# Kernel optimization log

Measured on AMD Instinct MI355X. Metric: run time of the kernel, lower is better.

## Reference

```python
import jax, jax.numpy as jnp
import numpy as np

# Config constants (MLAConfig)
B, S = 1, 2048                 # batch, context_len (prefill: seq == context_len)
H = 16                         # num_heads
DN, DR, DV = 128, 64, 128      # qk_nope_head_dim, qk_rope_head_dim, v_head_dim
QL, C = 1536, 512              # q_lora_rank, kv_lora_rank
BLK = 128                      # fp8 dequant block size
MAX_CACHE = 4096
SOFTMAX_SCALE = 1.0 / np.sqrt(DN + DR)  # 1/sqrt(192)
NEG_INF = -10000.0


def gen_rope(n_total, head_size):
    # theta_j = 10000^{-2j/d}; idx_theta[i, 0, :] = [i*theta, i*theta] (repeated halves)
    theta = 1.0 / (10000.0 ** (jnp.arange(0, head_size, 2, dtype=jnp.float32) / head_size))
    idx = jnp.outer(jnp.arange(n_total, dtype=jnp.float32), theta)  # (N, d/2)
    return jnp.tile(idx[:, None, :], (1, 1, 2))                     # (N, 1, d)


def fp8_dequant(x, s, block=BLK):
    # Block-wise dequant: x (M,N) * per-(block x block) scale s (M/b, N/b).
    M, N = x.shape
    m, n = M // block, N // block  # shapes chosen divisible by block -> no padding
    return (x.reshape(m, block, n, block) * s[:, None, :, None]).reshape(M, N)


def apply_rope(x, cos, sin):
    # x: (B*S, heads, d). Interleaved RoPE: de-interleave pairs into halves,
    # then x*cos + rotate_half(x)*sin with cos/sin (B*S, 1, d).
    bs, h, d = x.shape
    x = x.reshape(bs, h, d // 2, 2).transpose(0, 1, 3, 2).reshape(bs, h, d)
    rot = jnp.concatenate([-x[..., d // 2:], x[..., :d // 2]], axis=-1)
    return x * cos + rot * sin


def setup_inputs() -> dict:
    key = jax.random.key(0)
    ks = jax.random.split(key, 9)
    WUQ = jax.random.normal(ks[0], (H * (DN + DR), QL), dtype=jnp.float32)
    WUKV = jax.random.normal(ks[1], (H * (DN + DV), C), dtype=jnp.float32)
    # positive, small block scales so attention logits stay well-conditioned
    WUQ_scale = 0.05 * jax.random.uniform(ks[2], (H * (DN + DR) // BLK, QL // BLK), dtype=jnp.float32)
    WUKV_scale = 0.05 * jax.random.uniform(ks[3], (H * (DN + DV) // BLK, C // BLK), dtype=jnp.float32)
    Q = jax.random.normal(ks[4], (B, S, QL), dtype=jnp.float32)
    KV = jax.random.normal(ks[5], (B, S, C), dtype=jnp.float32)
    PE = jax.random.normal(ks[6], (B, S, DR), dtype=jnp.float32)
    kv_cache = jax.random.normal(ks[7], (B, MAX_CACHE, C), dtype=jnp.float32)
    pe_cache = jax.random.normal(ks[8], (B, MAX_CACHE, DR), dtype=jnp.float32)
    idx_theta = gen_rope(B * S, DR)
    mask = jnp.triu(jnp.full((S, S), NEG_INF, dtype=jnp.float32), k=1)
    return {"WUQ": WUQ, "WUQ_scale": WUQ_scale, "WUKV": WUKV, "WUKV_scale": WUKV_scale,
            "Q": Q, "KV": KV, "PE": PE, "kv_cache": kv_cache, "pe_cache": pe_cache,
            "idx_theta": idx_theta, "mask": mask}


def reference(WUQ, WUQ_scale, WUKV, WUKV_scale, Q, KV, PE, kv_cache, pe_cache, idx_theta, mask):
    bsz, seqlen, _ = Q.shape
    # fp8 block-wise dequant of the low-rank up-projection weights
    WUQd = fp8_dequant(WUQ, WUQ_scale)
    WUKVd = fp8_dequant(WUKV, WUKV_scale)
    # Q up-projection from q_lora latent: (B*S, QL) @ (QL, H*(DN+DR))
    q = (Q.reshape(-1, QL) @ WUQd.T).reshape(bsz, seqlen, H, DN + DR)
    q_nope, q_pe = q[..., :DN], q[..., DN:]
    cos, sin = jnp.cos(idx_theta), jnp.sin(idx_theta)  # (B*S, 1, DR)
    q_pe = apply_rope(q_pe.reshape(bsz * seqlen, H, DR), cos, sin).reshape(bsz, seqlen, H, DR)
    k_pe = apply_rope(PE.reshape(bsz * seqlen, 1, DR), cos, sin).reshape(bsz, seqlen, DR)
    # absorbed low-rank K matrix: q_nope projected into the kv latent space
    W3 = WUKVd.reshape(H, DN + DV, C)
    q_lat = jnp.einsum('bshd,hdc->bshc', q_nope, W3[:, :DN])
    # continuous-cache prefill: write fresh latents into the cache, attend over them
    kv = kv_cache.at[:, :seqlen].set(KV)[:, :seqlen]   # (B, S, C)
    pe = pe_cache.at[:, :seqlen].set(k_pe)[:, :seqlen]  # (B, S, DR)
    scores = (jnp.einsum('bshc,btc->bsht', q_lat, kv)
              + jnp.einsum('bshr,btr->bsht', q_pe, pe)) * SOFTMAX_SCALE
    scores = scores + mask[None, :, None, :]
    attn = jax.nn.softmax(scores, axis=-1)
    x = jnp.einsum('bsht,btc->bshc', attn, kv)
    out = jnp.einsum('bshc,hdc->bshd', x, W3[:, DN:])  # V up-projection (absorbed)
    return out  # (B, S, H, DV)
```

## Files before the change

kernel.cpp:

```cpp
#include <hip/hip_runtime.h>

typedef __bf16 bf16_t;
typedef __attribute__((ext_vector_type(4))) __bf16 bf16x4;
typedef __attribute__((ext_vector_type(8))) __bf16 bf16x8;
typedef __attribute__((ext_vector_type(4))) float f32x4;

#define SOFTMAX_SCALE 0.07216878364870322f
#define NEG_MASK (-10000.0f)
#define NEG_BIG  (-1e30f)

__device__ __forceinline__ void async16(const bf16_t* g, bf16_t* l) {
  __builtin_amdgcn_global_load_lds(
      (const __attribute__((address_space(1))) unsigned int*)g,
      (__attribute__((address_space(3))) unsigned int*)l, 16, 0, 0);
}


__global__ void k_rope_tables(const float* __restrict__ idxt,
                              float* __restrict__ cost, float* __restrict__ sint) {
  int i = blockIdx.x * 256 + threadIdx.x;
  float a = idxt[i];
  cost[i] = cosf(a);
  sint[i] = sinf(a);
}

__global__ void k_dequant(const float* __restrict__ W, const float* __restrict__ S,
                          bf16_t* __restrict__ out, int cols, int scols) {
  int i = (blockIdx.x * 256 + threadIdx.x) * 4;
  int r = i / cols, c = i % cols;
  float s = S[(r >> 7) * scols + (c >> 7)];
  float4 w = *(const float4*)(W + i);
  out[i + 0] = (bf16_t)(w.x * s);
  out[i + 1] = (bf16_t)(w.y * s);
  out[i + 2] = (bf16_t)(w.z * s);
  out[i + 3] = (bf16_t)(w.w * s);
}

__global__ void k_wv1t(const bf16_t* __restrict__ Wd, bf16_t* __restrict__ Wt) {
  int i = blockIdx.x * 256 + threadIdx.x;
  int c = i & 511, d = (i >> 9) & 127, h = i >> 16;
  Wt[(h << 16) + (c << 7) + d] = Wd[((h << 8) + d) * 512 + c];
}

__global__ void k_f32_to_bf16(const float* __restrict__ in, bf16_t* __restrict__ out) {
  int i = (blockIdx.x * 256 + threadIdx.x) * 4;
  float4 v = *(const float4*)(in + i);
  out[i + 0] = (bf16_t)v.x;
  out[i + 1] = (bf16_t)v.y;
  out[i + 2] = (bf16_t)v.z;
  out[i + 3] = (bf16_t)v.w;
}

__global__ void k_k4(const float* __restrict__ KV, bf16_t* __restrict__ K4) {
  int i = blockIdx.x * 256 + threadIdx.x;
  int c2 = i & 15, t = i >> 4;
  int tt = t >> 6, k = t & 63;
  const float* src = KV + (size_t)t * 512 + c2 * 32;
  bf16_t* dst = K4 + (size_t)tt * 36864 + c2 * 2048 + k * 8;
#pragma unroll
  for (int sub = 0; sub < 4; ++sub) {
    float4 u = *(const float4*)(src + sub * 8);
    float4 v = *(const float4*)(src + sub * 8 + 4);
    bf16x8 o;
    o[0] = (bf16_t)u.x; o[1] = (bf16_t)u.y; o[2] = (bf16_t)u.z; o[3] = (bf16_t)u.w;
    o[4] = (bf16_t)v.x; o[5] = (bf16_t)v.y; o[6] = (bf16_t)v.z; o[7] = (bf16_t)v.w;
    *(bf16x8*)(dst + sub * 512) = o;
  }
}

__global__ void k_v4(const float* __restrict__ KV, bf16_t* __restrict__ V4) {
  int i = blockIdx.x * 256 + threadIdx.x;
  int c = i & 511, a = i >> 9;
  int t0 = a * 8, tt = t0 >> 6;
  int key0 = t0 & 63, kk2 = key0 >> 5, sub = (key0 >> 3) & 3;
  bf16x8 o;
#pragma unroll
  for (int j = 0; j < 8; ++j)
    o[j] = (bf16_t)KV[(size_t)(t0 + j) * 512 + c];
  *(bf16x8*)(V4 + (size_t)tt * 32768 + kk2 * 16384 + sub * 4096 + c * 8) = o;
}

__global__ void k_pe_rope(const float* __restrict__ PE, const float* __restrict__ cost,
                          const float* __restrict__ sint, bf16_t* __restrict__ K4) {
  int i = blockIdx.x * 256 + threadIdx.x;
  int t = i >> 5, j = i & 31;
  float e = PE[t * 64 + 2 * j], o = PE[t * 64 + 2 * j + 1];
  float c1 = cost[t * 64 + j], s1 = sint[t * 64 + j];
  float c2 = cost[t * 64 + 32 + j], s2 = sint[t * 64 + 32 + j];
  int tt = t >> 6, k = t & 63;
  bf16_t* base = K4 + (size_t)tt * 36864 + (j >> 3) * 512 + k * 8 + (j & 7);
  base[16 * 2048] = (bf16_t)(e * c1 - o * s1);
  base[17 * 2048] = (bf16_t)(o * c2 + e * s2);
}

__global__ void k_q_rope(const bf16_t* __restrict__ q, const float* __restrict__ cost,
                         const float* __restrict__ sint, bf16_t* __restrict__ qfull) {
  int i = blockIdx.x * 256 + threadIdx.x;
  int j = i & 31, h = (i >> 5) & 15, t = i >> 9;
  const bf16_t* src = q + t * 3072 + h * 192 + 128;
  float e = (float)src[2 * j], o = (float)src[2 * j + 1];
  float c1 = cost[t * 64 + j], s1 = sint[t * 64 + j];
  float c2 = cost[t * 64 + 32 + j], s2 = sint[t * 64 + 32 + j];
  bf16_t* dst = qfull + (size_t)h * 2048 * 576 + t * 576 + 512;
  dst[j]      = (bf16_t)(e * c1 - o * s1);
  dst[32 + j] = (bf16_t)(o * c2 + e * s2);
}

template <int OUT_F32>
__global__ __launch_bounds__(256) void k_gemm(
    const bf16_t* __restrict__ A, int lda, long saz,
    const bf16_t* __restrict__ B, int ldb, long sbz,
    void* __restrict__ Cv, int ldc, long scz, int K) {
  __shared__ __attribute__((aligned(16))) bf16_t At[128 * 64];
  __shared__ __attribute__((aligned(16))) bf16_t Bt[128 * 64];
  const int tid = threadIdx.x;
  const int lane = tid & 63;
  const int wv = tid >> 6;
  const int fr = lane & 15, fq = lane >> 4;
  const int wm = (wv & 1) * 64, wn = (wv >> 1) * 64;
  const int m0 = blockIdx.x * 128, n0 = blockIdx.y * 128;
  const bf16_t* Ab = A + (long)blockIdx.z * saz;
  const bf16_t* Bb = B + (long)blockIdx.z * sbz;

  f32x4 acc[4][4] = {};
  bf16x8 va[4], vb[4];
#pragma unroll
  for (int j = 0; j < 4; ++j) {
    int ch = tid + j * 256, ar = ch >> 3, ac = (ch & 7) * 8;
    va[j] = *(const bf16x8*)(Ab + (size_t)(m0 + ar) * lda + ac);
    vb[j] = *(const bf16x8*)(Bb + (size_t)(n0 + ar) * ldb + ac);
  }

  for (int k0 = 0; k0 < K; k0 += 64) {
    __syncthreads();
#pragma unroll
    for (int j = 0; j < 4; ++j) {
      int ch = tid + j * 256, ar = ch >> 3, c8 = ch & 7;
      *(bf16x8*)(At + ar * 64 + ((c8 ^ (ar & 7)) * 8)) = va[j];
      *(bf16x8*)(Bt + ar * 64 + ((c8 ^ (ar & 7)) * 8)) = vb[j];
    }
    __syncthreads();
    if (k0 + 64 < K) {
#pragma unroll
      for (int j = 0; j < 4; ++j) {
        int ch = tid + j * 256, ar = ch >> 3, ac = (ch & 7) * 8;
        va[j] = *(const bf16x8*)(Ab + (size_t)(m0 + ar) * lda + k0 + 64 + ac);
        vb[j] = *(const bf16x8*)(Bb + (size_t)(n0 + ar) * ldb + k0 + 64 + ac);
      }
    }
#pragma unroll
    for (int kk = 0; kk < 2; ++kk) {
      bf16x8 af[4], bfr[4];
#pragma unroll
      for (int m = 0; m < 4; ++m)
        af[m] = *(const bf16x8*)(At + (wm + m * 16 + fr) * 64 + (((kk * 4 + fq) ^ (fr & 7)) * 8));
#pragma unroll
      for (int n = 0; n < 4; ++n)
        bfr[n] = *(const bf16x8*)(Bt + (wn + n * 16 + fr) * 64 + (((kk * 4 + fq) ^ (fr & 7)) * 8));
#pragma unroll
      for (int m = 0; m < 4; ++m)
#pragma unroll
        for (int n = 0; n < 4; ++n)
          acc[m][n] = __builtin_amdgcn_mfma_f32_16x16x32_bf16(af[m], bfr[n], acc[m][n], 0, 0, 0);
    }
  }
#pragma unroll
  for (int m = 0; m < 4; ++m) {
    int row = m0 + wm + m * 16 + fq * 4;
#pragma unroll
    for (int n = 0; n < 4; ++n) {
      int col = n0 + wn + n * 16 + fr;
#pragma unroll
      for (int i = 0; i < 4; ++i) {
        if (OUT_F32)
          ((float*)Cv)[(long)blockIdx.z * scz + (size_t)(row + i) * ldc + col] = acc[m][n][i];
        else
          ((bf16_t*)Cv)[(long)blockIdx.z * scz + (size_t)(row + i) * ldc + col] = (bf16_t)acc[m][n][i];
      }
    }
  }
}

__global__ __attribute__((amdgpu_flat_work_group_size(512, 512),
                          amdgpu_waves_per_eu(2, 2)))
void k_attn(const bf16_t* __restrict__ qfull,
            const bf16_t* __restrict__ K4,
            const bf16_t* __restrict__ V4,
            bf16_t* __restrict__ X) {
  __shared__ __attribute__((aligned(16))) bf16_t Kt[18 * 2048];
  __shared__ __attribute__((aligned(16))) bf16_t Vt[2 * 16384];
  __shared__ __attribute__((aligned(16))) bf16_t P[64 * 64];
  __shared__ __attribute__((aligned(16))) bf16_t Qpe[8 * 512];
  __shared__ float red[4][64];
  __shared__ float red2[4][64];
  __shared__ float rowm[2][64];
  __shared__ float rowl[2][64];
  __shared__ float alf[64];

  const int tid = threadIdx.x;
  const int lane = tid & 63;
  const int w = tid >> 6;
  const int fr = lane & 15, fq = lane >> 4;
  const int h = blockIdx.x & 15;
  const int qt = 31 - (blockIdx.x >> 4);
  const int nt = qt + 1;
  const int rg = w >> 2;
  const int kq = w & 3;

  const bf16_t* qh = qfull + (size_t)h * 2048 * 576;
  bf16_t* Xh = X + (size_t)h * 2048 * 512;

  if (tid < 64) { rowm[0][tid] = NEG_BIG; rowl[0][tid] = 0.f; }

  {
    int row = tid >> 3, sub = tid & 7;
    bf16x8 v = *(const bf16x8*)(qh + (size_t)(qt * 64 + row) * 576 + 512 + sub * 8);
    *(bf16x8*)(Qpe + sub * 512 + row * 8) = v;
  }

  bf16x8 qa[2][16];
  {
    const bf16_t* qb = qh + (size_t)(qt * 64 + rg * 32) * 576;
#pragma unroll
    for (int mf = 0; mf < 2; ++mf)
#pragma unroll
      for (int kk = 0; kk < 16; ++kk)
        qa[mf][kk] = *(const bf16x8*)(qb + (mf * 16 + fr) * 576 + kk * 32 + fq * 8);
  }

#pragma unroll
  for (int i = 0; i < 9; ++i) {
    int ck = w + 8 * i;
    async16(K4 + ck * 512 + lane * 8, Kt + ck * 512 + lane * 8);
  }

  f32x4 acc[2][8] = {};

  for (int t = 0; t < nt; ++t) {
    __syncthreads();

    {
      const bf16_t* vsrc = V4 + (size_t)t * 32768;
#pragma unroll
      for (int i = 0; i < 8; ++i) {
        int cv = w + 8 * i;
        async16(vsrc + cv * 512 + lane * 8, Vt + cv * 512 + lane * 8);
      }
    }

    f32x4 s[2] = {};
    __builtin_amdgcn_s_setprio(1);
#pragma unroll
    for (int kk = 0; kk < 16; ++kk) {
      bf16x8 kf = *(const bf16x8*)(Kt + kk * 2048 + fq * 512 + (kq * 16 + fr) * 8);
      s[0] = __builtin_amdgcn_mfma_f32_16x16x32_bf16(kf, qa[0][kk], s[0], 0, 0, 0);
      s[1] = __builtin_amdgcn_mfma_f32_16x16x32_bf16(kf, qa[1][kk], s[1], 0, 0, 0);
    }
#pragma unroll
    for (int kk = 16; kk < 18; ++kk) {
      bf16x8 kf = *(const bf16x8*)(Kt + kk * 2048 + fq * 512 + (kq * 16 + fr) * 8);
      bf16x8 q0 = *(const bf16x8*)(Qpe + ((kk - 16) * 4 + fq) * 512 + (rg * 32 + fr) * 8);
      bf16x8 q1 = *(const bf16x8*)(Qpe + ((kk - 16) * 4 + fq) * 512 + (rg * 32 + 16 + fr) * 8);
      s[0] = __builtin_amdgcn_mfma_f32_16x16x32_bf16(kf, q0, s[0], 0, 0, 0);
      s[1] = __builtin_amdgcn_mfma_f32_16x16x32_bf16(kf, q1, s[1], 0, 0, 0);
    }
    __builtin_amdgcn_s_setprio(0);

    bool diag = (t == qt);
#pragma unroll
    for (int mf = 0; mf < 2; ++mf) {
      int qrow = rg * 32 + mf * 16 + fr;
#pragma unroll
      for (int i = 0; i < 4; ++i) {
        float v = s[mf][i] * SOFTMAX_SCALE;
        if (diag) {
          int kcol = kq * 16 + fq * 4 + i;
          if (kcol > qrow) v += NEG_MASK;
        }
        s[mf][i] = v;
      }
      float km = fmaxf(fmaxf(s[mf][0], s[mf][1]), fmaxf(s[mf][2], s[mf][3]));
      km = fmaxf(km, __shfl_xor(km, 16));
      km = fmaxf(km, __shfl_xor(km, 32));
      if (fq == 0) red[kq][qrow] = km;
    }
    __syncthreads();

    float mnew[2], alpha[2];
#pragma unroll
    for (int mf = 0; mf < 2; ++mf) {
      int row = rg * 32 + mf * 16 + fr;
      float mt = fmaxf(fmaxf(red[0][row], red[1][row]), fmaxf(red[2][row], red[3][row]));
      float mo = rowm[t & 1][row];
      float mn = fmaxf(mo, mt);
      mnew[mf] = mn;
      alpha[mf] = __expf(mo - mn);
    }
#pragma unroll
    for (int mf = 0; mf < 2; ++mf) {
      int qrow = rg * 32 + mf * 16 + fr;
      float p0 = __expf(s[mf][0] - mnew[mf]);
      float p1 = __expf(s[mf][1] - mnew[mf]);
      float p2 = __expf(s[mf][2] - mnew[mf]);
      float p3 = __expf(s[mf][3] - mnew[mf]);
      bf16x4 pk;
      pk[0] = (bf16_t)p0; pk[1] = (bf16_t)p1; pk[2] = (bf16_t)p2; pk[3] = (bf16_t)p3;
      int chunk = (kq * 2 + (fq >> 1)) ^ (qrow & 7);
      *(bf16x4*)(P + qrow * 64 + chunk * 8 + (fq & 1) * 4) = pk;
      float rs = (p0 + p1) + (p2 + p3);
      rs += __shfl_xor(rs, 16);
      rs += __shfl_xor(rs, 32);
      if (fq == 0) red2[kq][qrow] = rs;
      if (kq == 0 && fq == 0) {
        alf[qrow] = alpha[mf];
        rowm[(t + 1) & 1][qrow] = mnew[mf];
      }
    }
    __syncthreads();

    if (t + 1 < nt) {
      const bf16_t* ksrc = K4 + (size_t)(t + 1) * 36864;
#pragma unroll
      for (int i = 0; i < 9; ++i) {
        int ck = w + 8 * i;
        async16(ksrc + ck * 512 + lane * 8, Kt + ck * 512 + lane * 8);
      }
    }

    if (kq == 0 && fq == 0) {
#pragma unroll
      for (int mf = 0; mf < 2; ++mf) {
        int row = rg * 32 + mf * 16 + fr;
        rowl[(t + 1) & 1][row] = rowl[t & 1][row] * alpha[mf] +
            ((red2[0][row] + red2[1][row]) + (red2[2][row] + red2[3][row]));
      }
    }

    f32x4 av[2];
#pragma unroll
    for (int mf = 0; mf < 2; ++mf)
      av[mf] = *(const f32x4*)(&alf[rg * 32 + mf * 16 + fq * 4]);
#pragma unroll
    for (int mf = 0; mf < 2; ++mf)
#pragma unroll
      for (int nf = 0; nf < 8; ++nf)
#pragma unroll
        for (int i = 0; i < 4; ++i) acc[mf][nf][i] *= av[mf][i];
    __builtin_amdgcn_s_setprio(1);
#pragma unroll
    for (int kk2 = 0; kk2 < 2; ++kk2) {
      bf16x8 pa[2];
#pragma unroll
      for (int mf = 0; mf < 2; ++mf) {
        int qrow = rg * 32 + mf * 16 + fr;
        pa[mf] = *(const bf16x8*)(P + qrow * 64 + (((kk2 * 4 + fq) ^ (qrow & 7)) * 8));
      }
#pragma unroll
      for (int nf = 0; nf < 8; ++nf) {
        bf16x8 vb = *(const bf16x8*)(Vt + kk2 * 16384 + fq * 4096 + (kq * 128 + nf * 16 + fr) * 8);
        acc[0][nf] = __builtin_amdgcn_mfma_f32_16x16x32_bf16(pa[0], vb, acc[0][nf], 0, 0, 0);
        acc[1][nf] = __builtin_amdgcn_mfma_f32_16x16x32_bf16(pa[1], vb, acc[1][nf], 0, 0, 0);
      }
    }
    __builtin_amdgcn_s_setprio(0);
  }

  __syncthreads();
  {
    bf16_t* XT = Kt;
#pragma unroll
    for (int mf = 0; mf < 2; ++mf)
#pragma unroll
      for (int i = 0; i < 4; ++i) {
        int row = rg * 32 + mf * 16 + fq * 4 + i;
        float invl = 1.0f / rowl[nt & 1][row];
#pragma unroll
        for (int nf = 0; nf < 8; ++nf)
          XT[row * 512 + kq * 128 + nf * 16 + fr] = (bf16_t)(acc[mf][nf][i] * invl);
      }
  }
  __syncthreads();
#pragma unroll
  for (int it = 0; it < 8; ++it) {
    int id = tid + it * 512;
    int row = id >> 6, j = id & 63;
    *(bf16x8*)(Xh + (size_t)(qt * 64 + row) * 512 + j * 8) = *(const bf16x8*)(Kt + row * 512 + j * 8);
  }
}


extern "C" void kernel_launch(void* const* d_in, const int* in_sizes, int n_in,
                              void* d_out, int out_size, void* d_ws, size_t ws_size,
                              hipStream_t stream) {
  (void)in_sizes; (void)n_in; (void)out_size; (void)ws_size;
  const float* WUQ   = (const float*)d_in[0];
  const float* WUQs  = (const float*)d_in[1];
  const float* WUKV  = (const float*)d_in[2];
  const float* WUKVs = (const float*)d_in[3];
  const float* Q     = (const float*)d_in[4];
  const float* KV    = (const float*)d_in[5];
  const float* PE    = (const float*)d_in[6];
  const float* idxt  = (const float*)d_in[9];
  float* out = (float*)d_out;

  char* ws = (char*)d_ws;
  size_t off = 0;
  auto alloc = [&](size_t n) -> char* {
    char* p = ws + off;
    off += (n + 255) & ~(size_t)255;
    return p;
  };
  float*  cost  = (float*)alloc((size_t)2048 * 64 * 4);
  float*  sint  = (float*)alloc((size_t)2048 * 64 * 4);
  bf16_t* WUQd  = (bf16_t*)alloc((size_t)3072 * 1536 * 2);
  bf16_t* WUKVd = (bf16_t*)alloc((size_t)4096 * 512 * 2);
  bf16_t* Wv1t  = (bf16_t*)alloc((size_t)16 * 512 * 128 * 2);
  bf16_t* Qb    = (bf16_t*)alloc((size_t)2048 * 1536 * 2);
  bf16_t* qbuf  = (bf16_t*)alloc((size_t)2048 * 3072 * 2);
  bf16_t* K4    = (bf16_t*)alloc((size_t)32 * 36864 * 2);
  bf16_t* V4    = (bf16_t*)alloc((size_t)32 * 32768 * 2);
  bf16_t* qfull = (bf16_t*)alloc((size_t)16 * 2048 * 576 * 2);
  bf16_t* Xb    = (bf16_t*)alloc((size_t)16 * 2048 * 512 * 2);

  k_rope_tables<<<512, 256, 0, stream>>>(idxt, cost, sint);
  k_dequant<<<4608, 256, 0, stream>>>(WUQ, WUQs, WUQd, 1536, 12);
  k_dequant<<<2048, 256, 0, stream>>>(WUKV, WUKVs, WUKVd, 512, 4);
  k_wv1t<<<4096, 256, 0, stream>>>(WUKVd, Wv1t);
  k_f32_to_bf16<<<3072, 256, 0, stream>>>(Q, Qb);
  k_k4<<<128, 256, 0, stream>>>(KV, K4);
  k_v4<<<512, 256, 0, stream>>>(KV, V4);
  k_pe_rope<<<256, 256, 0, stream>>>(PE, cost, sint, K4);
  k_gemm<0><<<dim3(16, 24, 1), 256, 0, stream>>>(Qb, 1536, 0, WUQd, 1536, 0,
                                                 qbuf, 3072, 0, 1536);
  k_q_rope<<<4096, 256, 0, stream>>>(qbuf, cost, sint, qfull);
  k_gemm<0><<<dim3(16, 4, 16), 256, 0, stream>>>(qbuf, 3072, 192, Wv1t, 128, (long)512 * 128,
                                                 qfull, 576, (long)2048 * 576, 128);
  k_attn<<<dim3(512), dim3(512), 0, stream>>>(qfull, K4, V4, Xb);
  k_gemm<1><<<dim3(16, 1, 16), 256, 0, stream>>>(Xb, 512, (long)2048 * 512,
                                                 WUKVd + 128 * 512, 512, (long)256 * 512,
                                                 out, 2048, 128, 512);
}
```

Baseline: 241.6 us.

## Fold softmax scale into Q conversion and use lazy online-softmax rescaling

Multiplies the softmax scale into the bf16 conversion of the query operand so the attention loop no longer scales every score. Adds a threshold-based lazy rescale: the running max is only updated when a tile's max exceeds it by more than 8, and the accumulator rescale is skipped wave-wide when no row needs it. This removes per-tile exp and multiply work on the 64 accumulator registers, at the cost of larger unnormalized exponent ranges (up to e^8), a divergent branch, and a rounding change from scaling before bf16 conversion.

```diff
diff --git a/kernel.cpp b/kernel.cpp
--- a/kernel.cpp
+++ b/kernel.cpp
@@ -8,6 +8,7 @@
 #define SOFTMAX_SCALE 0.07216878364870322f
 #define NEG_MASK (-10000.0f)
 #define NEG_BIG  (-1e30f)
+#define RESCALE_THR 8.0f
 
 __device__ __forceinline__ void async16(const bf16_t* g, bf16_t* l) {
   __builtin_amdgcn_global_load_lds(
@@ -45,10 +46,10 @@
 __global__ void k_f32_to_bf16(const float* __restrict__ in, bf16_t* __restrict__ out) {
   int i = (blockIdx.x * 256 + threadIdx.x) * 4;
   float4 v = *(const float4*)(in + i);
-  out[i + 0] = (bf16_t)v.x;
-  out[i + 1] = (bf16_t)v.y;
-  out[i + 2] = (bf16_t)v.z;
-  out[i + 3] = (bf16_t)v.w;
+  out[i + 0] = (bf16_t)(v.x * SOFTMAX_SCALE);
+  out[i + 1] = (bf16_t)(v.y * SOFTMAX_SCALE);
+  out[i + 2] = (bf16_t)(v.z * SOFTMAX_SCALE);
+  out[i + 3] = (bf16_t)(v.w * SOFTMAX_SCALE);
 }
 
 __global__ void k_k4(const float* __restrict__ KV, bf16_t* __restrict__ K4) {
@@ -270,14 +271,12 @@
 #pragma unroll
     for (int mf = 0; mf < 2; ++mf) {
       int qrow = rg * 32 + mf * 16 + fr;
-#pragma unroll
-      for (int i = 0; i < 4; ++i) {
-        float v = s[mf][i] * SOFTMAX_SCALE;
-        if (diag) {
+      if (diag) {
+#pragma unroll
+        for (int i = 0; i < 4; ++i) {
           int kcol = kq * 16 + fq * 4 + i;
-          if (kcol > qrow) v += NEG_MASK;
+          if (kcol > qrow) s[mf][i] += NEG_MASK;
         }
-        s[mf][i] = v;
       }
       float km = fmaxf(fmaxf(s[mf][0], s[mf][1]), fmaxf(s[mf][2], s[mf][3]));
       km = fmaxf(km, __shfl_xor(km, 16));
@@ -286,23 +285,21 @@
     }
     __syncthreads();
 
-    float mnew[2], alpha[2];
+    float mnew[2];
 #pragma unroll
     for (int mf = 0; mf < 2; ++mf) {
       int row = rg * 32 + mf * 16 + fr;
       float mt = fmaxf(fmaxf(red[0][row], red[1][row]), fmaxf(red[2][row], red[3][row]));
       float mo = rowm[t & 1][row];
-      float mn = fmaxf(mo, mt);
+      bool grow = mt > mo + RESCALE_THR;
+      float mn = grow ? mt : mo;
       mnew[mf] = mn;
-      alpha[mf] = __expf(mo - mn);
-    }
-#pragma unroll
-    for (int mf = 0; mf < 2; ++mf) {
-      int qrow = rg * 32 + mf * 16 + fr;
-      float p0 = __expf(s[mf][0] - mnew[mf]);
-      float p1 = __expf(s[mf][1] - mnew[mf]);
-      float p2 = __expf(s[mf][2] - mnew[mf]);
-      float p3 = __expf(s[mf][3] - mnew[mf]);
+      float alpha = grow ? __expf(mo - mn) : 1.0f;
+      int qrow = row;
+      float p0 = __expf(s[mf][0] - mn);
+      float p1 = __expf(s[mf][1] - mn);
+      float p2 = __expf(s[mf][2] - mn);
+      float p3 = __expf(s[mf][3] - mn);
       bf16x4 pk;
       pk[0] = (bf16_t)p0; pk[1] = (bf16_t)p1; pk[2] = (bf16_t)p2; pk[3] = (bf16_t)p3;
       int chunk = (kq * 2 + (fq >> 1)) ^ (qrow & 7);
@@ -312,8 +309,8 @@
       rs += __shfl_xor(rs, 32);
       if (fq == 0) red2[kq][qrow] = rs;
       if (kq == 0 && fq == 0) {
-        alf[qrow] = alpha[mf];
-        rowm[(t + 1) & 1][qrow] = mnew[mf];
+        alf[qrow] = alpha;
+        rowm[(t + 1) & 1][qrow] = mn;
       }
     }
     __syncthreads();
@@ -331,7 +328,7 @@
 #pragma unroll
       for (int mf = 0; mf < 2; ++mf) {
         int row = rg * 32 + mf * 16 + fr;
-        rowl[(t + 1) & 1][row] = rowl[t & 1][row] * alpha[mf] +
+        rowl[(t + 1) & 1][row] = rowl[t & 1][row] * alf[row] +
             ((red2[0][row] + red2[1][row]) + (red2[2][row] + red2[3][row]));
       }
     }
@@ -340,12 +337,19 @@
 #pragma unroll
     for (int mf = 0; mf < 2; ++mf)
       av[mf] = *(const f32x4*)(&alf[rg * 32 + mf * 16 + fq * 4]);
+    int need = 0;
 #pragma unroll
     for (int mf = 0; mf < 2; ++mf)
 #pragma unroll
-      for (int nf = 0; nf < 8; ++nf)
-#pragma unroll
-        for (int i = 0; i < 4; ++i) acc[mf][nf][i] *= av[mf][i];
+      for (int i = 0; i < 4; ++i) need |= (av[mf][i] != 1.0f);
+    if (__any(need)) {
+#pragma unroll
+      for (int mf = 0; mf < 2; ++mf)
+#pragma unroll
+        for (int nf = 0; nf < 8; ++nf)
+#pragma unroll
+          for (int i = 0; i < 4; ++i) acc[mf][nf][i] *= av[mf][i];
+    }
     __builtin_amdgcn_s_setprio(1);
 #pragma unroll
     for (int kk2 = 0; kk2 < 2; ++kk2) {
```

Result: no change. 239.1 us (-1.0%).
